# Optimization experiments

Measured on AMD Instinct MI355X. Metric: run time of the kernel, lower is better.

The kernel has to match this reference:

```python
import jax, jax.numpy as jnp
import numpy as np

N_FREQ = 7  # freqs = 2**linspace(0, 6, 7) == 2**arange(7)
SKIP = (4,)


def nerf_encode(p):
    # nerfstudio NeRFEncoding with include_input=True, windows_param=None
    freqs = 2.0 ** jnp.arange(N_FREQ, dtype=p.dtype)          # [7]
    scaled = (2.0 * jnp.pi) * p                               # [N,3]
    s = (scaled[..., None] * freqs).reshape(p.shape[0], -1)   # [N,21]
    enc = jnp.sin(jnp.concatenate([s, s + 0.5 * jnp.pi], axis=-1))  # [N,42] = sin | cos
    return jnp.concatenate([enc, p], axis=-1)                 # [N,45]


def _hat_pt3d(w):
    # pytorch3d hat convention (transpose of the standard skew matrix)
    x, y, z = w[:, 0], w[:, 1], w[:, 2]
    o = jnp.zeros_like(x)
    return jnp.stack([
        jnp.stack([o, z, -y], -1),
        jnp.stack([-z, o, x], -1),
        jnp.stack([y, -x, o], -1)], -2)                       # [N,3,3]


def se3_exp_map_T(screw, eps=1e-4):
    # pytorch3d.transforms.se3_exp_map(screw).permute(0, 2, 1)
    v, w = screw[:, :3], screw[:, 3:]
    ang2 = jnp.clip(jnp.sum(w * w, axis=-1), eps, None)
    ang = jnp.sqrt(ang2)
    K = _hat_pt3d(w)
    KK = jnp.matmul(K, K)
    f1 = (jnp.sin(ang) / ang)[:, None, None]
    f2 = ((1.0 - jnp.cos(ang)) / ang2)[:, None, None]
    f3 = ((ang - jnp.sin(ang)) / (ang * ang2))[:, None, None]
    I = jnp.eye(3, dtype=screw.dtype)
    R = I + f1 * K + f2 * KK       # pytorch3d (row-vector) rotation
    V = I + f2 * K + f3 * KK
    T = jnp.einsum('nij,nj->ni', V, v)
    M = jnp.zeros((screw.shape[0], 4, 4), screw.dtype)
    M = M.at[:, :3, :3].set(jnp.swapaxes(R, -1, -2))  # transpose of [[R,0],[T,1]]
    M = M.at[:, :3, 3].set(T)
    M = M.at[:, 3, 3].set(1.0)
    return M


def mlp_stem(x, Ws, bs):
    inp = x
    n = len(Ws)
    for i in range(n):
        if i in SKIP:
            x = jnp.concatenate([inp, x], axis=-1)
        x = x @ Ws[i].T + bs[i]
        x = jax.nn.relu(x)  # hidden activation; i==n-1 is out_activation (also ReLU)
    return x


def setup_inputs() -> dict:
    key = jax.random.key(0)
    ks = jax.random.split(key, 16)
    N = 524288
    d = {
        'positions': jax.random.uniform(ks[0], (N, 3), jnp.float32),
        'directions': jax.random.normal(ks[1], (N, 3), jnp.float32),
        'warp_code': jax.random.normal(ks[2], (N, 8), jnp.float32),
    }
    fan_ins = [53, 128, 128, 128, 181, 128]
    for i, fi in enumerate(fan_ins):
        d[f'W{i}'] = jax.random.normal(ks[3 + i], (128, fi), jnp.float32) / np.sqrt(fi)
        d[f'b{i}'] = jnp.zeros((128,), jnp.float32)
    d['Wr'] = jax.random.normal(ks[10], (3, 128), jnp.float32) * 1e-5
    d['br'] = jnp.zeros((3,), jnp.float32)
    d['Wv'] = jax.random.normal(ks[11], (3, 128), jnp.float32) * 1e-5
    d['bv'] = jnp.zeros((3,), jnp.float32)
    return d


def reference(positions, directions, warp_code,
              W0, b0, W1, b1, W2, b2, W3, b3, W4, b4, W5, b5,
              Wr, br, Wv, bv):
    enc = nerf_encode(positions)                                  # [N,45]
    feat = mlp_stem(jnp.concatenate([enc, warp_code], axis=-1),
                    [W0, W1, W2, W3, W4, W5], [b0, b1, b2, b3, b4, b5])  # [N,128]
    r = feat @ Wr.T + br                                          # [N,3]
    v = feat @ Wv.T + bv                                          # [N,3]
    screw = jnp.concatenate([v, r], axis=-1)                      # [N,6]
    M = se3_exp_map_T(screw)                                      # [N,4,4]
    ph = jnp.concatenate([positions, jnp.ones_like(positions[:, :1])], axis=-1)
    wp_h = jnp.einsum('nij,nj->ni', M, ph)                        # [N,4]
    wp = wp_h[:, :3] / wp_h[:, 3:]
    wp = jnp.where(jnp.isnan(wp), positions, wp)
    rots = M[:, :3, :3]
    wd = jnp.einsum('nij,nj->ni', rots, directions)
    wd = jnp.where(jnp.isnan(wd), directions, wd)
    return wp, wd
```

## Files before the change

kernel.cpp:

```cpp
#include <hip/hip_runtime.h>
#include <hip/hip_bf16.h>
#include <math.h>


typedef __bf16 bf16x8 __attribute__((ext_vector_type(8)));
typedef float  f32x4  __attribute__((ext_vector_type(4)));

#define NROWS 524288
#define BROWS 128

#define P0 0
#define P1 8192
#define P2 24576
#define P3 40960
#define P4 57344
#define P5 81920
#define PH 98304
#define PTOT 100352

#define X0_OFF 0
#define XA_OFF 16384
#define XB_OFF 49152
#define SC_OFF 16384
#define LDS_SZ 81920

__global__ void pack_w(const float* __restrict__ W0, const float* __restrict__ W1,
                       const float* __restrict__ W2, const float* __restrict__ W3,
                       const float* __restrict__ W4, const float* __restrict__ W5,
                       const float* __restrict__ Wr, const float* __restrict__ Wv,
                       __bf16* __restrict__ pk)
{
    int e = blockIdx.x * 256 + threadIdx.x;
    if (e >= PTOT) return;
    float val = 0.f;
    if (e >= PH) {
        int rem = e - PH;
        int s = rem >> 9, r3 = rem & 511, ln = r3 >> 3, j = r3 & 7;
        int col = ln & 15;
        int k = s * 32 + (ln >> 4) * 8 + j;
        if (col < 3)      val = Wv[col * 128 + k];
        else if (col < 6) val = Wr[(col - 3) * 128 + k];
        else              val = 0.f;
    } else {
        const float* W; int KS, base, fan;
        if (e < P1)      { W = W0; KS = 2; base = P0; fan = 53;  }
        else if (e < P2) { W = W1; KS = 4; base = P1; fan = 128; }
        else if (e < P3) { W = W2; KS = 4; base = P2; fan = 128; }
        else if (e < P4) { W = W3; KS = 4; base = P3; fan = 128; }
        else if (e < P5) { W = W4; KS = 6; base = P4; fan = 181; }
        else             { W = W5; KS = 4; base = P5; fan = 128; }
        int rem = e - base;
        int perf = KS * 512;
        int f = rem / perf, r2 = rem % perf;
        int s = r2 >> 9, r3 = r2 & 511, ln = r3 >> 3, j = r3 & 7;
        int col = f * 16 + (ln & 15);
        int k = s * 32 + (ln >> 4) * 8 + j;
        if (fan == 128)     val = W[col * 128 + k];
        else if (fan == 53) val = (k < 53) ? W[col * 53 + k] : 0.f;
        else {
            if (k < 53)      val = W[col * 181 + k];
            else if (k < 64) val = 0.f;
            else             val = W[col * 181 + (k - 11)];
        }
    }
    pk[e] = (__bf16)val;
}

__global__ __launch_bounds__(256, 2)
void se3_fused(const float* __restrict__ pos, const float* __restrict__ dir,
               const float* __restrict__ wcode,
               const float* __restrict__ b0, const float* __restrict__ b1,
               const float* __restrict__ b2, const float* __restrict__ b3,
               const float* __restrict__ b4, const float* __restrict__ b5,
               const float* __restrict__ br, const float* __restrict__ bv,
               const __bf16* __restrict__ pk,
               float* __restrict__ out)
{
    __shared__ unsigned char smem[LDS_SZ];
    const int tid  = threadIdx.x;
    const int lane = tid & 63;
    const int cl   = lane & 15;
    const int gp   = lane >> 4;
    const int wid  = tid >> 6;
    const int r0   = blockIdx.x * BROWS;

    {
        int row = tid >> 1, h = tid & 1;
        int g = r0 + row;
        float p3[3] = { pos[g*3+0], pos[g*3+1], pos[g*3+2] };
        unsigned char* base = smem + X0_OFF + row * 128;
        int sw = (row & 7) << 4;
        auto put = [&](int col, float v) {
            *(__bf16*)(base + ((col * 2) ^ sw)) = (__bf16)v;
        };
        if (h == 0) {
            #pragma unroll
            for (int a = 0; a < 3; a++)
                #pragma unroll
                for (int f = 0; f < 4; f++) {
                    float t = p3[a] * (float)(1 << f);
                    t -= floorf(t);
                    float ang = 6.283185307179586f * t;
                    put(a*7+f,      __sinf(ang));
                    put(21+a*7+f,   __cosf(ang));
                }
        } else {
            #pragma unroll
            for (int a = 0; a < 3; a++)
                #pragma unroll
                for (int f = 4; f < 7; f++) {
                    float t = p3[a] * (float)(1 << f);
                    t -= floorf(t);
                    float ang = 6.283185307179586f * t;
                    put(a*7+f,      __sinf(ang));
                    put(21+a*7+f,   __cosf(ang));
                }
            put(42, p3[0]); put(43, p3[1]); put(44, p3[2]);
            #pragma unroll
            for (int j = 0; j < 8; j++) put(45+j, wcode[g*8+j]);
            #pragma unroll
            for (int c = 53; c < 64; c++) put(c, 0.f);
        }
    }
    __syncthreads();

    auto layer = [&](int KS, int splitS, int inOff, int inStride,
                     int pkOff, const float* bias, int outOff) {
        f32x4 acc[8][2];
        float bb0 = bias[wid*32 + cl];
        float bb1 = bias[wid*32 + 16 + cl];
        #pragma unroll
        for (int rf = 0; rf < 8; rf++) {
            acc[rf][0] = f32x4{bb0, bb0, bb0, bb0};
            acc[rf][1] = f32x4{bb1, bb1, bb1, bb1};
        }
        const bf16x8* pB = (const bf16x8*)(pk + pkOff);
        for (int s = 0; s < KS; s++) {
            bf16x8 Bf0 = pB[((wid*2)     * KS + s) * 64 + lane];
            bf16x8 Bf1 = pB[((wid*2 + 1) * KS + s) * 64 + lane];
            int bbase, bstride, kloc;
            if (s < splitS) { bbase = X0_OFF; bstride = 128;      kloc = s * 32; }
            else            { bbase = inOff;  bstride = inStride; kloc = (s - splitS) * 32; }
            int kb = kloc * 2 + gp * 16;
            #pragma unroll
            for (int rf = 0; rf < 8; rf++) {
                int row = rf * 16 + cl;
                bf16x8 A = *(const bf16x8*)(smem + bbase + row * bstride
                                            + (kb ^ ((row & 7) << 4)));
                acc[rf][0] = __builtin_amdgcn_mfma_f32_16x16x32_bf16(A, Bf0, acc[rf][0], 0, 0, 0);
                acc[rf][1] = __builtin_amdgcn_mfma_f32_16x16x32_bf16(A, Bf1, acc[rf][1], 0, 0, 0);
            }
        }
        #pragma unroll
        for (int rf = 0; rf < 8; rf++)
            #pragma unroll
            for (int cf = 0; cf < 2; cf++) {
                int cb = ((wid*2 + cf) * 16 + cl) * 2;
                #pragma unroll
                for (int r = 0; r < 4; r++) {
                    int row = rf * 16 + gp * 4 + r;
                    float v = acc[rf][cf][r];
                    v = v > 0.f ? v : 0.f;
                    *(__bf16*)(smem + outOff + row * 256 + (cb ^ ((row & 7) << 4))) = (__bf16)v;
                }
            }
        __syncthreads();
    };

    layer(2, 0, X0_OFF, 128, P0, b0, XA_OFF);
    layer(4, 0, XA_OFF, 256, P1, b1, XB_OFF);
    layer(4, 0, XB_OFF, 256, P2, b2, XA_OFF);
    layer(4, 0, XA_OFF, 256, P3, b3, XB_OFF);
    layer(6, 2, XB_OFF, 256, P4, b4, XA_OFF);
    layer(4, 0, XA_OFF, 256, P5, b5, XB_OFF);

    {
        f32x4 ha[2];
        float hb = (cl < 3) ? bv[cl] : ((cl < 6) ? br[cl - 3] : 0.f);
        ha[0] = f32x4{hb, hb, hb, hb};
        ha[1] = f32x4{hb, hb, hb, hb};
        const bf16x8* pB = (const bf16x8*)(pk + PH);
        #pragma unroll
        for (int s = 0; s < 4; s++) {
            bf16x8 Bf = pB[s * 64 + lane];
            int kb = s * 64 + gp * 16;
            #pragma unroll
            for (int q = 0; q < 2; q++) {
                int row = (wid*2 + q) * 16 + cl;
                bf16x8 A = *(const bf16x8*)(smem + XB_OFF + row * 256
                                            + (kb ^ ((row & 7) << 4)));
                ha[q] = __builtin_amdgcn_mfma_f32_16x16x32_bf16(A, Bf, ha[q], 0, 0, 0);
            }
        }
        if (cl < 6) {
            #pragma unroll
            for (int q = 0; q < 2; q++)
                #pragma unroll
                for (int r = 0; r < 4; r++) {
                    int row = (wid*2 + q) * 16 + gp * 4 + r;
                    *(float*)(smem + SC_OFF + row * 32 + cl * 4) = ha[q][r];
                }
        }
    }
    __syncthreads();

    if (tid < BROWS) {
        int row = tid, g = r0 + row;
        const float* sc = (const float*)(smem + SC_OFF + row * 32);
        float v0 = sc[0], v1 = sc[1], v2 = sc[2];
        float wx = sc[3], wy = sc[4], wz = sc[5];
        float ang2 = wx*wx + wy*wy + wz*wz;
        ang2 = fmaxf(ang2, 1e-4f);
        float ang = sqrtf(ang2);
        float sn = __sinf(ang), cs = __cosf(ang);
        float f1 = sn / ang;
        float f2 = (1.f - cs) / ang2;
        float f3 = (ang - sn) / (ang * ang2);
        float K[3][3] = {{0.f,  wz, -wy}, {-wz, 0.f,  wx}, { wy, -wx, 0.f}};
        float KK[3][3];
        #pragma unroll
        for (int i = 0; i < 3; i++)
            #pragma unroll
            for (int j = 0; j < 3; j++)
                KK[i][j] = K[i][0]*K[0][j] + K[i][1]*K[1][j] + K[i][2]*K[2][j];
        float R[3][3], V[3][3];
        #pragma unroll
        for (int i = 0; i < 3; i++)
            #pragma unroll
            for (int j = 0; j < 3; j++) {
                float id = (i == j) ? 1.f : 0.f;
                R[i][j] = id + f1 * K[i][j] + f2 * KK[i][j];
                V[i][j] = id + f2 * K[i][j] + f3 * KK[i][j];
            }
        float T0 = V[0][0]*v0 + V[0][1]*v1 + V[0][2]*v2;
        float T1 = V[1][0]*v0 + V[1][1]*v1 + V[1][2]*v2;
        float T2 = V[2][0]*v0 + V[2][1]*v1 + V[2][2]*v2;
        float px = pos[g*3+0], py = pos[g*3+1], pz = pos[g*3+2];
        float dx = dir[g*3+0], dy = dir[g*3+1], dz = dir[g*3+2];
        float wpx = R[0][0]*px + R[1][0]*py + R[2][0]*pz + T0;
        float wpy = R[0][1]*px + R[1][1]*py + R[2][1]*pz + T1;
        float wpz = R[0][2]*px + R[1][2]*py + R[2][2]*pz + T2;
        float wdx = R[0][0]*dx + R[1][0]*dy + R[2][0]*dz;
        float wdy = R[0][1]*dx + R[1][1]*dy + R[2][1]*dz;
        float wdz = R[0][2]*dx + R[1][2]*dy + R[2][2]*dz;
        wpx = (wpx != wpx) ? px : wpx;
        wpy = (wpy != wpy) ? py : wpy;
        wpz = (wpz != wpz) ? pz : wpz;
        wdx = (wdx != wdx) ? dx : wdx;
        wdy = (wdy != wdy) ? dy : wdy;
        wdz = (wdz != wdz) ? dz : wdz;
        out[g*3+0] = wpx; out[g*3+1] = wpy; out[g*3+2] = wpz;
        float* o2 = out + (size_t)NROWS * 3;
        o2[g*3+0] = wdx; o2[g*3+1] = wdy; o2[g*3+2] = wdz;
    }
}

extern "C" void kernel_launch(void* const* d_in, const int* in_sizes, int n_in,
                              void* d_out, int out_size, void* d_ws, size_t ws_size,
                              hipStream_t stream)
{
    const float* pos = (const float*)d_in[0];
    const float* dir = (const float*)d_in[1];
    const float* wc  = (const float*)d_in[2];
    const float* W0 = (const float*)d_in[3];  const float* b0 = (const float*)d_in[4];
    const float* W1 = (const float*)d_in[5];  const float* b1 = (const float*)d_in[6];
    const float* W2 = (const float*)d_in[7];  const float* b2 = (const float*)d_in[8];
    const float* W3 = (const float*)d_in[9];  const float* b3 = (const float*)d_in[10];
    const float* W4 = (const float*)d_in[11]; const float* b4 = (const float*)d_in[12];
    const float* W5 = (const float*)d_in[13]; const float* b5 = (const float*)d_in[14];
    const float* Wr = (const float*)d_in[15]; const float* br = (const float*)d_in[16];
    const float* Wv = (const float*)d_in[17]; const float* bv = (const float*)d_in[18];
    __bf16* pk = (__bf16*)d_ws;
    float* out = (float*)d_out;

    pack_w<<<(PTOT + 255) / 256, 256, 0, stream>>>(W0, W1, W2, W3, W4, W5, Wr, Wv, pk);
    se3_fused<<<NROWS / BROWS, 256, 0, stream>>>(pos, dir, wc,
                                                 b0, b1, b2, b3, b4, b5,
                                                 br, bv, pk, out);
}
```

Baseline: 239.8 us.

## Retile MLP layers as 2x2 wave grid with in-place LDS and prefetch

Each MLP layer is restructured so the four waves form a 2x2 grid over output features and rows, computing the transposed product (weights as A, activations as B). This lets each wave load four weight fragments and four activation fragments per k-step instead of two and eight. The K loop is fully unrolled and double-buffers the next step's weight and activation fragments. Layers now write in place to a single activation buffer, with a barrier before the write, which frees the second buffer, shrinks LDS to 48 KB and raises launch bounds to three blocks per SM. Outputs are written as packed bf16 pairs, and the head GEMM runs on half the waves. The gains in occupancy and fewer LDS reads come at the cost of higher register pressure and an extra barrier per layer.

```diff
diff --git a/kernel.cpp b/kernel.cpp
--- a/kernel.cpp
+++ b/kernel.cpp
@@ -20,9 +20,8 @@
 
 #define X0_OFF 0
 #define XA_OFF 16384
-#define XB_OFF 49152
-#define SC_OFF 16384
-#define LDS_SZ 81920
+#define SC_OFF 0
+#define LDS_SZ 49152
 
 __global__ void pack_w(const float* __restrict__ W0, const float* __restrict__ W1,
                        const float* __restrict__ W2, const float* __restrict__ W3,
@@ -66,7 +65,77 @@
     pk[e] = (__bf16)val;
 }
 
-__global__ __launch_bounds__(256, 2)
+__device__ __forceinline__ unsigned pack_bf16_2(float a, float b) {
+    union { __bf16 h; unsigned short u; } x, y;
+    x.h = (__bf16)a; y.h = (__bf16)b;
+    return ((unsigned)y.u << 16) | (unsigned)x.u;
+}
+
+template<int KS, int SPLITS>
+__device__ __forceinline__ void mlp_layer(unsigned char* smem,
+    const __bf16* __restrict__ pkL, const float* __restrict__ bias,
+    int inOff, int inStride, int outOff,
+    int lane, int cl, int gp, int mfG, int nfG)
+{
+    const bf16x8* pW = (const bf16x8*)pkL;
+
+    f32x4 acc[4][4];
+    #pragma unroll
+    for (int mf = 0; mf < 4; mf++) {
+        f32x4 bb = *(const f32x4*)(bias + mfG * 64 + mf * 16 + gp * 4);
+        #pragma unroll
+        for (int nf = 0; nf < 4; nf++) acc[mf][nf] = bb;
+    }
+
+    bf16x8 Wf[2][4], Bf[2][4];
+    auto loadW = [&](bf16x8* dst, int s) {
+        #pragma unroll
+        for (int mf = 0; mf < 4; mf++)
+            dst[mf] = pW[((mfG * 4 + mf) * KS + s) * 64 + lane];
+    };
+    auto loadB = [&](bf16x8* dst, int s) {
+        int base, stride, k0;
+        if (s < SPLITS) { base = X0_OFF; stride = 128;      k0 = s * 32; }
+        else            { base = inOff;  stride = inStride; k0 = (s - SPLITS) * 32; }
+        int bc = 2 * k0 + 16 * gp;
+        #pragma unroll
+        for (int nf = 0; nf < 4; nf++) {
+            int row = nfG * 64 + nf * 16 + cl;
+            dst[nf] = *(const bf16x8*)(smem + base + row * stride
+                                       + (bc ^ ((row & 7) << 4)));
+        }
+    };
+
+    loadW(Wf[0], 0);
+    loadB(Bf[0], 0);
+    #pragma unroll
+    for (int s = 0; s < KS; s++) {
+        if (s + 1 < KS) { loadW(Wf[(s + 1) & 1], s + 1); loadB(Bf[(s + 1) & 1], s + 1); }
+        #pragma unroll
+        for (int mf = 0; mf < 4; mf++)
+            #pragma unroll
+            for (int nf = 0; nf < 4; nf++)
+                acc[mf][nf] = __builtin_amdgcn_mfma_f32_16x16x32_bf16(
+                    Wf[s & 1][mf], Bf[s & 1][nf], acc[mf][nf], 0, 0, 0);
+    }
+
+    __syncthreads();
+    #pragma unroll
+    for (int mf = 0; mf < 4; mf++)
+        #pragma unroll
+        for (int nf = 0; nf < 4; nf++) {
+            int row = nfG * 64 + nf * 16 + cl;
+            int bc  = 128 * mfG + 32 * mf + 8 * gp;
+            f32x4 a = acc[mf][nf];
+            uint2 w;
+            w.x = pack_bf16_2(fmaxf(a[0], 0.f), fmaxf(a[1], 0.f));
+            w.y = pack_bf16_2(fmaxf(a[2], 0.f), fmaxf(a[3], 0.f));
+            *(uint2*)(smem + outOff + row * 256 + (bc ^ ((row & 7) << 4))) = w;
+        }
+    __syncthreads();
+}
+
+__global__ __launch_bounds__(256, 3)
 void se3_fused(const float* __restrict__ pos, const float* __restrict__ dir,
                const float* __restrict__ wcode,
                const float* __restrict__ b0, const float* __restrict__ b1,
@@ -82,6 +151,8 @@
     const int cl   = lane & 15;
     const int gp   = lane >> 4;
     const int wid  = tid >> 6;
+    const int mfG  = wid & 1;
+    const int nfG  = wid >> 1;
     const int r0   = blockIdx.x * BROWS;
 
     {
@@ -124,82 +195,45 @@
     }
     __syncthreads();
 
-    auto layer = [&](int KS, int splitS, int inOff, int inStride,
-                     int pkOff, const float* bias, int outOff) {
-        f32x4 acc[8][2];
-        float bb0 = bias[wid*32 + cl];
-        float bb1 = bias[wid*32 + 16 + cl];
-        #pragma unroll
-        for (int rf = 0; rf < 8; rf++) {
-            acc[rf][0] = f32x4{bb0, bb0, bb0, bb0};
-            acc[rf][1] = f32x4{bb1, bb1, bb1, bb1};
-        }
-        const bf16x8* pB = (const bf16x8*)(pk + pkOff);
-        for (int s = 0; s < KS; s++) {
-            bf16x8 Bf0 = pB[((wid*2)     * KS + s) * 64 + lane];
-            bf16x8 Bf1 = pB[((wid*2 + 1) * KS + s) * 64 + lane];
-            int bbase, bstride, kloc;
-            if (s < splitS) { bbase = X0_OFF; bstride = 128;      kloc = s * 32; }
-            else            { bbase = inOff;  bstride = inStride; kloc = (s - splitS) * 32; }
-            int kb = kloc * 2 + gp * 16;
-            #pragma unroll
-            for (int rf = 0; rf < 8; rf++) {
-                int row = rf * 16 + cl;
-                bf16x8 A = *(const bf16x8*)(smem + bbase + row * bstride
-                                            + (kb ^ ((row & 7) << 4)));
-                acc[rf][0] = __builtin_amdgcn_mfma_f32_16x16x32_bf16(A, Bf0, acc[rf][0], 0, 0, 0);
-                acc[rf][1] = __builtin_amdgcn_mfma_f32_16x16x32_bf16(A, Bf1, acc[rf][1], 0, 0, 0);
+    mlp_layer<2,0>(smem, pk + P0, b0, X0_OFF, 128, XA_OFF, lane, cl, gp, mfG, nfG);
+    mlp_layer<4,0>(smem, pk + P1, b1, XA_OFF, 256, XA_OFF, lane, cl, gp, mfG, nfG);
+    mlp_layer<4,0>(smem, pk + P2, b2, XA_OFF, 256, XA_OFF, lane, cl, gp, mfG, nfG);
+    mlp_layer<4,0>(smem, pk + P3, b3, XA_OFF, 256, XA_OFF, lane, cl, gp, mfG, nfG);
+    mlp_layer<6,2>(smem, pk + P4, b4, XA_OFF, 256, XA_OFF, lane, cl, gp, mfG, nfG);
+    mlp_layer<4,0>(smem, pk + P5, b5, XA_OFF, 256, XA_OFF, lane, cl, gp, mfG, nfG);
+
+    if (mfG == 0) {
+        const bf16x8* pW = (const bf16x8*)(pk + PH);
+        f32x4 hb;
+        #pragma unroll
+        for (int r = 0; r < 4; r++) {
+            int m = gp * 4 + r;
+            hb[r] = (m < 3) ? bv[m] : ((m < 6) ? br[m - 3] : 0.f);
+        }
+        f32x4 hacc[4];
+        #pragma unroll
+        for (int nf = 0; nf < 4; nf++) hacc[nf] = hb;
+        #pragma unroll
+        for (int s = 0; s < 4; s++) {
+            bf16x8 Wh = pW[s * 64 + lane];
+            int bc = 64 * s + 16 * gp;
+            #pragma unroll
+            for (int nf = 0; nf < 4; nf++) {
+                int row = nfG * 64 + nf * 16 + cl;
+                bf16x8 B = *(const bf16x8*)(smem + XA_OFF + row * 256
+                                            + (bc ^ ((row & 7) << 4)));
+                hacc[nf] = __builtin_amdgcn_mfma_f32_16x16x32_bf16(Wh, B, hacc[nf], 0, 0, 0);
             }
         }
         #pragma unroll
-        for (int rf = 0; rf < 8; rf++)
-            #pragma unroll
-            for (int cf = 0; cf < 2; cf++) {
-                int cb = ((wid*2 + cf) * 16 + cl) * 2;
-                #pragma unroll
-                for (int r = 0; r < 4; r++) {
-                    int row = rf * 16 + gp * 4 + r;
-                    float v = acc[rf][cf][r];
-                    v = v > 0.f ? v : 0.f;
-                    *(__bf16*)(smem + outOff + row * 256 + (cb ^ ((row & 7) << 4))) = (__bf16)v;
-                }
+        for (int nf = 0; nf < 4; nf++) {
+            int row = nfG * 64 + nf * 16 + cl;
+            if (gp == 0) {
+                *(f32x4*)(smem + SC_OFF + row * 32) = hacc[nf];
+            } else if (gp == 1) {
+                *(float*)(smem + SC_OFF + row * 32 + 16) = hacc[nf][0];
+                *(float*)(smem + SC_OFF + row * 32 + 20) = hacc[nf][1];
             }
-        __syncthreads();
-    };
-
-    layer(2, 0, X0_OFF, 128, P0, b0, XA_OFF);
-    layer(4, 0, XA_OFF, 256, P1, b1, XB_OFF);
-    layer(4, 0, XB_OFF, 256, P2, b2, XA_OFF);
-    layer(4, 0, XA_OFF, 256, P3, b3, XB_OFF);
-    layer(6, 2, XB_OFF, 256, P4, b4, XA_OFF);
-    layer(4, 0, XA_OFF, 256, P5, b5, XB_OFF);
-
-    {
-        f32x4 ha[2];
-        float hb = (cl < 3) ? bv[cl] : ((cl < 6) ? br[cl - 3] : 0.f);
-        ha[0] = f32x4{hb, hb, hb, hb};
-        ha[1] = f32x4{hb, hb, hb, hb};
-        const bf16x8* pB = (const bf16x8*)(pk + PH);
-        #pragma unroll
-        for (int s = 0; s < 4; s++) {
-            bf16x8 Bf = pB[s * 64 + lane];
-            int kb = s * 64 + gp * 16;
-            #pragma unroll
-            for (int q = 0; q < 2; q++) {
-                int row = (wid*2 + q) * 16 + cl;
-                bf16x8 A = *(const bf16x8*)(smem + XB_OFF + row * 256
-                                            + (kb ^ ((row & 7) << 4)));
-                ha[q] = __builtin_amdgcn_mfma_f32_16x16x32_bf16(A, Bf, ha[q], 0, 0, 0);
-            }
-        }
-        if (cl < 6) {
-            #pragma unroll
-            for (int q = 0; q < 2; q++)
-                #pragma unroll
-                for (int r = 0; r < 4; r++) {
-                    int row = (wid*2 + q) * 16 + gp * 4 + r;
-                    *(float*)(smem + SC_OFF + row * 32 + cl * 4) = ha[q][r];
-                }
         }
     }
     __syncthreads();
```

Measured after the change: 221.9 us. 7.5% less time.
